# Kernel tuning notes

Measured on AMD Instinct MI355X. Metric: run time of the kernel, lower is better.

The kernel has to match this reference:

```python
import jax, jax.numpy as jnp
import numpy as np

N_EMBED = 1024
N_HEADS = 16
HEAD = N_EMBED // N_HEADS
EPS = 1e-5


def setup_inputs() -> dict:
    key = jax.random.key(0)
    ks = jax.random.split(key, 16)
    C = N_EMBED
    s = lambda fan_in: 1.0 / np.sqrt(fan_in)
    return {
        "x": jax.random.normal(ks[0], (4, 2048, C), jnp.float32),
        "ln1_g": jnp.ones((C,), jnp.float32),
        "ln1_b": jnp.zeros((C,), jnp.float32),
        "w_attn": jax.random.normal(ks[1], (C, 3 * C), jnp.float32) * s(C),
        "b_attn": jnp.zeros((3 * C,), jnp.float32),
        "w_proj": jax.random.normal(ks[2], (C, C), jnp.float32) * s(C),
        "b_proj": jnp.zeros((C,), jnp.float32),
        "ln2_g": jnp.ones((C,), jnp.float32),
        "ln2_b": jnp.zeros((C,), jnp.float32),
        "w_fc": jax.random.normal(ks[3], (C, 4 * C), jnp.float32) * s(C),
        "b_fc": jnp.zeros((4 * C,), jnp.float32),
        "w_fc2": jax.random.normal(ks[4], (4 * C, C), jnp.float32) * s(4 * C),
        "b_fc2": jnp.zeros((C,), jnp.float32),
    }


def _layernorm(x, g, b):
    mu = jnp.mean(x, axis=-1, keepdims=True)
    var = jnp.mean(jnp.square(x - mu), axis=-1, keepdims=True)
    return (x - mu) * jax.lax.rsqrt(var + EPS) * g + b


def _attention(x, w_attn, b_attn, w_proj, b_proj):
    B, T, C = x.shape
    qkv = x @ w_attn + b_attn  # [B,T,3C]
    q, k, v = jnp.split(qkv, 3, axis=-1)
    q = q.reshape(B, T, N_HEADS, HEAD).transpose(0, 2, 1, 3)  # [B,H,T,D]
    k = k.reshape(B, T, N_HEADS, HEAD).transpose(0, 2, 1, 3)
    v = v.reshape(B, T, N_HEADS, HEAD).transpose(0, 2, 1, 3)
    scale = 1.0 / np.sqrt(HEAD)
    affin = jnp.einsum("bhqd,bhkd->bhqk", q, k) * scale  # [B,H,T,T]
    causal = jnp.tril(jnp.ones((T, T), bool))
    affin = jnp.where(causal, affin, -jnp.inf)
    affin = jax.nn.softmax(affin, axis=-1)
    y = jnp.einsum("bhqk,bhkd->bhqd", affin, v)  # [B,H,T,D]
    y = y.transpose(0, 2, 1, 3).reshape(B, T, C)
    return y @ w_proj + b_proj


def reference(x, ln1_g, ln1_b, w_attn, b_attn, w_proj, b_proj,
              ln2_g, ln2_b, w_fc, b_fc, w_fc2, b_fc2):
    x = x + _attention(_layernorm(x, ln1_g, ln1_b), w_attn, b_attn, w_proj, b_proj)
    h = _layernorm(x, ln2_g, ln2_b)
    h = jax.nn.gelu(h @ w_fc + b_fc, approximate=True)  # tanh GELU
    x = x + (h @ w_fc2 + b_fc2)
    return x
```

## Files before the change

kernel.cpp:

```cpp
#include <hip/hip_runtime.h>
#include <math.h>


#define M_ROWS 8192
#define T_SEQ 2048
#define N_EMB 1024
#define N_HEADS 16
#define HEAD_D 64

typedef _Float16 f16;
typedef __attribute__((ext_vector_type(8))) _Float16 f16x8;
typedef __attribute__((ext_vector_type(4))) _Float16 f16x4;
typedef __attribute__((ext_vector_type(4))) float f32x4;

__device__ __forceinline__ void async16(void* lds, const void* g) {
    __builtin_amdgcn_global_load_lds(
        (const __attribute__((address_space(1))) unsigned int*)g,
        (__attribute__((address_space(3))) unsigned int*)lds, 16, 0, 0);
}

__device__ __forceinline__ float gelu_tanh(float v) {
    float u = 0.7978845608028654f * (v + 0.044715f * v * v * v);
    float e = __expf(2.0f * u);
    float t = 1.0f - 2.0f / (e + 1.0f);
    return 0.5f * v * (1.0f + t);
}

__launch_bounds__(256)
__global__ void wconv_kernel(const float* __restrict__ W, f16* __restrict__ WT,
                             int K, int N) {
    __shared__ float t[32][33];
    int tx = threadIdx.x & 31, ty = threadIdx.x >> 5;
    int n0 = blockIdx.x * 32, k0 = blockIdx.y * 32;
    #pragma unroll
    for (int r = 0; r < 4; r++)
        t[ty * 4 + r][tx] = W[(size_t)(k0 + ty * 4 + r) * N + n0 + tx];
    __syncthreads();
    #pragma unroll
    for (int r = 0; r < 4; r++)
        WT[(size_t)(n0 + ty * 4 + r) * K + k0 + tx] = (f16)t[tx][ty * 4 + r];
}

__launch_bounds__(256)
__global__ void ln_kernel(const float* __restrict__ x, const float* __restrict__ g,
                          const float* __restrict__ b, f16* __restrict__ y) {
    int row = blockIdx.x;
    int tid = threadIdx.x;
    const float* xr = x + (size_t)row * N_EMB;
    float4 v = *(const float4*)(xr + tid * 4);
    float s  = v.x + v.y + v.z + v.w;
    float sq = v.x * v.x + v.y * v.y + v.z * v.z + v.w * v.w;
    #pragma unroll
    for (int off = 32; off > 0; off >>= 1) {
        s  += __shfl_down(s, off);
        sq += __shfl_down(sq, off);
    }
    __shared__ float ws_[4], wq_[4];
    __shared__ float mean_s, rstd_s;
    int lane = tid & 63, wid = tid >> 6;
    if (lane == 0) { ws_[wid] = s; wq_[wid] = sq; }
    __syncthreads();
    if (tid == 0) {
        float st = ws_[0] + ws_[1] + ws_[2] + ws_[3];
        float qt = wq_[0] + wq_[1] + wq_[2] + wq_[3];
        float mu = st * (1.0f / N_EMB);
        float var = qt * (1.0f / N_EMB) - mu * mu;
        mean_s = mu;
        rstd_s = rsqrtf(var + 1e-5f);
    }
    __syncthreads();
    float mu = mean_s, r = rstd_s;
    float4 gv = *(const float4*)(g + tid * 4);
    float4 bv = *(const float4*)(b + tid * 4);
    f16x4 o;
    o.x = (f16)((v.x - mu) * r * gv.x + bv.x);
    o.y = (f16)((v.y - mu) * r * gv.y + bv.y);
    o.z = (f16)((v.z - mu) * r * gv.z + bv.z);
    o.w = (f16)((v.w - mu) * r * gv.w + bv.w);
    *(f16x4*)(y + (size_t)row * N_EMB + tid * 4) = o;
}

template <int EPI>
__launch_bounds__(256)
__global__ void gemm_f16(const f16* __restrict__ A, const f16* __restrict__ Bt,
                         const float* __restrict__ bias, const float* __restrict__ res,
                         float* __restrict__ Cf, f16* __restrict__ Ch,
                         f16* __restrict__ vT, int K, int N) {
    __shared__ f16 As[128 * 32];
    __shared__ f16 Bs[128 * 32];
    int tid = threadIdx.x;
    int lane = tid & 63, wave = tid >> 6;
    int wr = wave >> 1, wc = wave & 1;
    int quad = lane >> 4, l16 = lane & 15;
    int m0 = blockIdx.y * 128, n0 = blockIdx.x * 128;

    f32x4 acc[4][4] = {};

    for (int k0 = 0; k0 < K; k0 += 32) {
        #pragma unroll
        for (int i = 0; i < 2; i++) {
            int L = i * 256 + tid;
            int row = L >> 2, seg = L & 3;
            async16((char*)As + (size_t)L * 16,
                    A + (size_t)(m0 + row) * K + k0 + seg * 8);
        }
        #pragma unroll
        for (int i = 0; i < 2; i++) {
            int L = i * 256 + tid;
            int row = L >> 2, seg = L & 3;
            async16((char*)Bs + (size_t)L * 16,
                    Bt + (size_t)(n0 + row) * K + k0 + seg * 8);
        }
        __syncthreads();

        f16x8 af[4], bf[4];
        #pragma unroll
        for (int i = 0; i < 4; i++)
            af[i] = *(const f16x8*)&As[(wr * 64 + i * 16 + l16) * 32 + quad * 8];
        #pragma unroll
        for (int j = 0; j < 4; j++)
            bf[j] = *(const f16x8*)&Bs[(wc * 64 + j * 16 + l16) * 32 + quad * 8];
        #pragma unroll
        for (int i = 0; i < 4; i++)
            #pragma unroll
            for (int j = 0; j < 4; j++)
                acc[i][j] = __builtin_amdgcn_mfma_f32_16x16x32_f16(
                    af[i], bf[j], acc[i][j], 0, 0, 0);
        __syncthreads();
    }

    #pragma unroll
    for (int i = 0; i < 4; i++) {
        int row0 = m0 + wr * 64 + i * 16 + quad * 4;
        #pragma unroll
        for (int j = 0; j < 4; j++) {
            int col = n0 + wc * 64 + j * 16 + l16;
            float bb = bias[col];
            if (EPI == 3) {
                if (n0 < 2048) {
                    #pragma unroll
                    for (int r = 0; r < 4; r++)
                        Ch[(size_t)(row0 + r) * 2048 + col] = (f16)(acc[i][j][r] + bb);
                } else {
                    int hh = (col - 2048) >> 6, dd = col & 63;
                    int bb_ = row0 >> 11, t0 = row0 & 2047;
                    f16x4 pk;
                    pk.x = (f16)(acc[i][j][0] + bb);
                    pk.y = (f16)(acc[i][j][1] + bb);
                    pk.z = (f16)(acc[i][j][2] + bb);
                    pk.w = (f16)(acc[i][j][3] + bb);
                    *(f16x4*)(vT + ((size_t)(bb_ * 16 + hh) * 64 + dd) * 2048 + t0) = pk;
                }
            } else {
                #pragma unroll
                for (int r = 0; r < 4; r++) {
                    size_t idx = (size_t)(row0 + r) * N + col;
                    float v = acc[i][j][r] + bb;
                    if (EPI == 1) v += res[idx];
                    if (EPI == 2) Ch[idx] = (f16)gelu_tanh(v);
                    else          Cf[idx] = v;
                }
            }
        }
    }
}

__launch_bounds__(256, 2)
__global__ void flash_kernel(const f16* __restrict__ qk, const f16* __restrict__ vT,
                             f16* __restrict__ y) {
    __shared__ __align__(16) char smem[67584];
    f16* Ks = (f16*)smem;
    f16* Vs = (f16*)(smem + 16384);
    int tid = threadIdx.x;
    int lane = tid & 63, w = tid >> 6;
    int quad = lane >> 4, l16 = lane & 15;
    f16* Ps = (f16*)(smem + 32768 + w * 8704);

    int qt = 15 - blockIdx.x;
    int bh = blockIdx.y;
    int b = bh >> 4, h = bh & 15;
    int q0 = qt * 128;

    f16x8 qf[2][2];
    #pragma unroll
    for (int qn = 0; qn < 2; qn++) {
        int q = q0 + w * 32 + qn * 16 + l16;
        #pragma unroll
        for (int dblk = 0; dblk < 2; dblk++)
            qf[qn][dblk] = *(const f16x8*)(qk + (size_t)(b * T_SEQ + q) * 2048 +
                                           h * 64 + dblk * 32 + quad * 8);
    }

    float m_r[2] = {-INFINITY, -INFINITY};
    float l_r[2] = {0.0f, 0.0f};
    f32x4 Oacc[2][4] = {};
    const float scale = 0.125f;

    for (int jt = 0; jt <= qt; jt++) {
        int j0 = jt * 128;
        __syncthreads();
        #pragma unroll
        for (int i = 0; i < 4; i++) {
            int L = i * 256 + tid;
            int j = L >> 3, g1 = L & 7;
            int g = g1 ^ (j & 7);
            async16((char*)Ks + (size_t)L * 16,
                    qk + (size_t)(b * T_SEQ + j0 + j) * 2048 + 1024 + h * 64 + g * 8);
        }
        #pragma unroll
        for (int i = 0; i < 4; i++) {
            int L = i * 256 + tid;
            int d = L >> 4, g1 = L & 15;
            int g = (g1 & 8) | ((g1 ^ d) & 7);
            async16((char*)Vs + (size_t)L * 16,
                    vT + ((size_t)(bh) * 64 + d) * 2048 + j0 + g * 8);
        }
        __syncthreads();

        f32x4 S[8][2];
        #pragma unroll
        for (int jm = 0; jm < 8; jm++) {
            f16x8 kf[2];
            #pragma unroll
            for (int dblk = 0; dblk < 2; dblk++) {
                int j = jm * 16 + l16;
                int g = (dblk * 4 + quad) ^ (j & 7);
                kf[dblk] = *(const f16x8*)(Ks + (size_t)(j * 8 + g) * 8);
            }
            #pragma unroll
            for (int qn = 0; qn < 2; qn++) {
                f32x4 s = {};
                s = __builtin_amdgcn_mfma_f32_16x16x32_f16(kf[0], qf[qn][0], s, 0, 0, 0);
                s = __builtin_amdgcn_mfma_f32_16x16x32_f16(kf[1], qf[qn][1], s, 0, 0, 0);
                S[jm][qn] = s;
            }
        }

        if (jt == qt) {
            #pragma unroll
            for (int jm = 0; jm < 8; jm++)
                #pragma unroll
                for (int qn = 0; qn < 2; qn++)
                    #pragma unroll
                    for (int r = 0; r < 4; r++) {
                        int jl = jm * 16 + quad * 4 + r;
                        int ql = w * 32 + qn * 16 + l16;
                        if (jl > ql) S[jm][qn][r] = -1e30f;
                    }
        }

        float alpha[2];
        #pragma unroll
        for (int qn = 0; qn < 2; qn++) {
            float tmax = -INFINITY;
            #pragma unroll
            for (int jm = 0; jm < 8; jm++)
                #pragma unroll
                for (int r = 0; r < 4; r++)
                    tmax = fmaxf(tmax, S[jm][qn][r]);
            tmax = fmaxf(tmax, __shfl_xor(tmax, 16));
            tmax = fmaxf(tmax, __shfl_xor(tmax, 32));
            tmax *= scale;
            float mnew = fmaxf(m_r[qn], tmax);
            alpha[qn] = __expf(m_r[qn] - mnew);
            m_r[qn] = mnew;
            float rsum = 0.0f;
            #pragma unroll
            for (int jm = 0; jm < 8; jm++)
                #pragma unroll
                for (int r = 0; r < 4; r++) {
                    float p = __expf(S[jm][qn][r] * scale - mnew);
                    S[jm][qn][r] = p;
                    rsum += p;
                }
            rsum += __shfl_xor(rsum, 16);
            rsum += __shfl_xor(rsum, 32);
            l_r[qn] = l_r[qn] * alpha[qn] + rsum;
        }

        #pragma unroll
        for (int jm = 0; jm < 8; jm++)
            #pragma unroll
            for (int qn = 0; qn < 2; qn++) {
                f16x4 pk;
                pk.x = (f16)S[jm][qn][0];
                pk.y = (f16)S[jm][qn][1];
                pk.z = (f16)S[jm][qn][2];
                pk.w = (f16)S[jm][qn][3];
                *(f16x4*)(Ps + (size_t)(qn * 16 + l16) * 136 + jm * 16 + quad * 4) = pk;
            }

        float aPV[2][4];
        #pragma unroll
        for (int m = 0; m < 2; m++)
            #pragma unroll
            for (int r = 0; r < 4; r++)
                aPV[m][r] = __shfl(alpha[m], quad * 20 + r);
        #pragma unroll
        for (int m = 0; m < 2; m++)
            #pragma unroll
            for (int n = 0; n < 4; n++)
                #pragma unroll
                for (int r = 0; r < 4; r++)
                    Oacc[m][n][r] *= aPV[m][r];

        #pragma unroll
        for (int kblk = 0; kblk < 4; kblk++) {
            f16x8 pf[2];
            #pragma unroll
            for (int m = 0; m < 2; m++)
                pf[m] = *(const f16x8*)(Ps + (size_t)(m * 16 + l16) * 136 +
                                        kblk * 32 + quad * 8);
            f16x8 vf[4];
            #pragma unroll
            for (int n = 0; n < 4; n++) {
                int d = n * 16 + l16;
                int g = (kblk * 4 + quad);
                int gs = (g & 8) | ((g ^ d) & 7);
                vf[n] = *(const f16x8*)(Vs + (size_t)(d * 16 + gs) * 8);
            }
            #pragma unroll
            for (int m = 0; m < 2; m++)
                #pragma unroll
                for (int n = 0; n < 4; n++)
                    Oacc[m][n] = __builtin_amdgcn_mfma_f32_16x16x32_f16(
                        pf[m], vf[n], Oacc[m][n], 0, 0, 0);
        }
    }

    #pragma unroll
    for (int m = 0; m < 2; m++) {
        float lPV[4];
        #pragma unroll
        for (int r = 0; r < 4; r++)
            lPV[r] = 1.0f / __shfl(l_r[m], quad * 20 + r);
        #pragma unroll
        for (int n = 0; n < 4; n++) {
            #pragma unroll
            for (int r = 0; r < 4; r++) {
                int q = q0 + w * 32 + m * 16 + quad * 4 + r;
                y[(size_t)(b * T_SEQ + q) * N_EMB + h * 64 + n * 16 + l16] =
                    (f16)(Oacc[m][n][r] * lPV[r]);
            }
        }
    }
}

extern "C" void kernel_launch(void* const* d_in, const int* in_sizes, int n_in,
                              void* d_out, int out_size, void* d_ws, size_t ws_size,
                              hipStream_t stream) {
    const float* x      = (const float*)d_in[0];
    const float* ln1_g  = (const float*)d_in[1];
    const float* ln1_b  = (const float*)d_in[2];
    const float* w_attn = (const float*)d_in[3];
    const float* b_attn = (const float*)d_in[4];
    const float* w_proj = (const float*)d_in[5];
    const float* b_proj = (const float*)d_in[6];
    const float* ln2_g  = (const float*)d_in[7];
    const float* ln2_b  = (const float*)d_in[8];
    const float* w_fc   = (const float*)d_in[9];
    const float* b_fc   = (const float*)d_in[10];
    const float* w_fc2  = (const float*)d_in[11];
    const float* b_fc2  = (const float*)d_in[12];
    float* out = (float*)d_out;

    const size_t MB = 1024 * 1024;
    char* ws = (char*)d_ws;
    f16*   lnbuf = (f16*)ws;
    f16*   qkbuf = (f16*)(ws + 16 * MB);
    f16*   vTbuf = (f16*)(ws + 48 * MB);
    f16*   ybuf  = (f16*)(ws + 64 * MB);
    f16*   h     = (f16*)(ws + 80 * MB);
    f16*   wT    = (f16*)(ws + 144 * MB);
    f16* wT_attn = wT;
    f16* wT_proj = wT_attn + (size_t)3072 * 1024;
    f16* wT_fc   = wT_proj + (size_t)1024 * 1024;
    f16* wT_fc2  = wT_fc   + (size_t)1024 * 4096;

    wconv_kernel<<<dim3(3072 / 32, 1024 / 32), 256, 0, stream>>>(w_attn, wT_attn, 1024, 3072);
    wconv_kernel<<<dim3(1024 / 32, 1024 / 32), 256, 0, stream>>>(w_proj, wT_proj, 1024, 1024);
    wconv_kernel<<<dim3(4096 / 32, 1024 / 32), 256, 0, stream>>>(w_fc,   wT_fc,   1024, 4096);
    wconv_kernel<<<dim3(1024 / 32, 4096 / 32), 256, 0, stream>>>(w_fc2,  wT_fc2,  4096, 1024);

    ln_kernel<<<M_ROWS, 256, 0, stream>>>(x, ln1_g, ln1_b, lnbuf);
    gemm_f16<3><<<dim3(3072 / 128, M_ROWS / 128), 256, 0, stream>>>(
        lnbuf, wT_attn, b_attn, nullptr, nullptr, qkbuf, vTbuf, 1024, 3072);
    flash_kernel<<<dim3(16, 64), 256, 0, stream>>>(qkbuf, vTbuf, ybuf);
    gemm_f16<1><<<dim3(1024 / 128, M_ROWS / 128), 256, 0, stream>>>(
        ybuf, wT_proj, b_proj, x, out, nullptr, nullptr, 1024, 1024);
    ln_kernel<<<M_ROWS, 256, 0, stream>>>(out, ln2_g, ln2_b, lnbuf);
    gemm_f16<2><<<dim3(4096 / 128, M_ROWS / 128), 256, 0, stream>>>(
        lnbuf, wT_fc, b_fc, nullptr, nullptr, h, nullptr, 1024, 4096);
    gemm_f16<1><<<dim3(1024 / 128, M_ROWS / 128), 256, 0, stream>>>(
        h, wT_fc2, b_fc2, out, out, nullptr, nullptr, 4096, 1024);
}
```

Before: 609.6 us.

## Swizzle GEMM LDS tiles, transpose MFMA output for vector epilogue, prescale Q

New measurement: 639.7 us. 4.9% more time.

```diff
diff --git a/kernel.cpp b/kernel.cpp
--- a/kernel.cpp
+++ b/kernel.cpp
@@ -96,70 +96,85 @@
 
     f32x4 acc[4][4] = {};
 
+    int srowA[2], ssegA[2];
+    #pragma unroll
+    for (int i = 0; i < 2; i++) {
+        int L = i * 256 + tid;
+        int row = L >> 2, seg = L & 3;
+        srowA[i] = row;
+        ssegA[i] = seg ^ (row & 3) ^ ((row >> 2) & 3);
+    }
+    int r2 = (l16 & 3) ^ (l16 >> 2);
+
     for (int k0 = 0; k0 < K; k0 += 32) {
         #pragma unroll
         for (int i = 0; i < 2; i++) {
             int L = i * 256 + tid;
-            int row = L >> 2, seg = L & 3;
             async16((char*)As + (size_t)L * 16,
-                    A + (size_t)(m0 + row) * K + k0 + seg * 8);
+                    A + (size_t)(m0 + srowA[i]) * K + k0 + ssegA[i] * 8);
         }
         #pragma unroll
         for (int i = 0; i < 2; i++) {
             int L = i * 256 + tid;
-            int row = L >> 2, seg = L & 3;
             async16((char*)Bs + (size_t)L * 16,
-                    Bt + (size_t)(n0 + row) * K + k0 + seg * 8);
+                    Bt + (size_t)(n0 + srowA[i]) * K + k0 + ssegA[i] * 8);
         }
         __syncthreads();
 
         f16x8 af[4], bf[4];
         #pragma unroll
         for (int i = 0; i < 4; i++)
-            af[i] = *(const f16x8*)&As[(wr * 64 + i * 16 + l16) * 32 + quad * 8];
+            af[i] = *(const f16x8*)&As[(size_t)((wr * 64 + i * 16 + l16) * 4 +
+                                                (quad ^ r2)) * 8];
         #pragma unroll
         for (int j = 0; j < 4; j++)
-            bf[j] = *(const f16x8*)&Bs[(wc * 64 + j * 16 + l16) * 32 + quad * 8];
+            bf[j] = *(const f16x8*)&Bs[(size_t)((wc * 64 + j * 16 + l16) * 4 +
+                                                (quad ^ r2)) * 8];
         #pragma unroll
         for (int i = 0; i < 4; i++)
             #pragma unroll
             for (int j = 0; j < 4; j++)
                 acc[i][j] = __builtin_amdgcn_mfma_f32_16x16x32_f16(
-                    af[i], bf[j], acc[i][j], 0, 0, 0);
+                    bf[j], af[i], acc[i][j], 0, 0, 0);
         __syncthreads();
     }
 
     #pragma unroll
     for (int i = 0; i < 4; i++) {
-        int row0 = m0 + wr * 64 + i * 16 + quad * 4;
+        int m = m0 + wr * 64 + i * 16 + l16;
         #pragma unroll
         for (int j = 0; j < 4; j++) {
-            int col = n0 + wc * 64 + j * 16 + l16;
-            float bb = bias[col];
+            int nb = n0 + wc * 64 + j * 16 + quad * 4;
+            float4 bb = *(const float4*)(bias + nb);
+            float v0 = acc[i][j][0] + bb.x;
+            float v1 = acc[i][j][1] + bb.y;
+            float v2 = acc[i][j][2] + bb.z;
+            float v3 = acc[i][j][3] + bb.w;
             if (EPI == 3) {
                 if (n0 < 2048) {
-                    #pragma unroll
-                    for (int r = 0; r < 4; r++)
-                        Ch[(size_t)(row0 + r) * 2048 + col] = (f16)(acc[i][j][r] + bb);
+                    f16x4 pk = {(f16)v0, (f16)v1, (f16)v2, (f16)v3};
+                    *(f16x4*)(Ch + (size_t)m * 2048 + nb) = pk;
                 } else {
-                    int hh = (col - 2048) >> 6, dd = col & 63;
-                    int bb_ = row0 >> 11, t0 = row0 & 2047;
-                    f16x4 pk;
-                    pk.x = (f16)(acc[i][j][0] + bb);
-                    pk.y = (f16)(acc[i][j][1] + bb);
-                    pk.z = (f16)(acc[i][j][2] + bb);
-                    pk.w = (f16)(acc[i][j][3] + bb);
-                    *(f16x4*)(vT + ((size_t)(bb_ * 16 + hh) * 64 + dd) * 2048 + t0) = pk;
+                    int hh = (nb - 2048) >> 6, d0 = nb & 63;
+                    int b_ = m >> 11, t0 = m & 2047;
+                    f16* vbase = vT + ((size_t)(b_ * 16 + hh) * 64 + d0) * 2048 + t0;
+                    vbase[0]        = (f16)v0;
+                    vbase[2048]     = (f16)v1;
+                    vbase[2 * 2048] = (f16)v2;
+                    vbase[3 * 2048] = (f16)v3;
                 }
+            } else if (EPI == 2) {
+                f16x4 pk = {(f16)gelu_tanh(v0), (f16)gelu_tanh(v1),
+                            (f16)gelu_tanh(v2), (f16)gelu_tanh(v3)};
+                *(f16x4*)(Ch + (size_t)m * N + nb) = pk;
             } else {
-                #pragma unroll
-                for (int r = 0; r < 4; r++) {
-                    size_t idx = (size_t)(row0 + r) * N + col;
-                    float v = acc[i][j][r] + bb;
-                    if (EPI == 1) v += res[idx];
-                    if (EPI == 2) Ch[idx] = (f16)gelu_tanh(v);
-                    else          Cf[idx] = v;
+                size_t idx = (size_t)m * N + nb;
+                if (EPI == 1) {
+                    float4 rr = *(const float4*)(res + idx);
+                    v0 += rr.x; v1 += rr.y; v2 += rr.z; v3 += rr.w;
                 }
+                float4 ov = {v0, v1, v2, v3};
+                *(float4*)(Cf + idx) = ov;
             }
         }
     }
@@ -186,15 +201,18 @@
     for (int qn = 0; qn < 2; qn++) {
         int q = q0 + w * 32 + qn * 16 + l16;
         #pragma unroll
-        for (int dblk = 0; dblk < 2; dblk++)
-            qf[qn][dblk] = *(const f16x8*)(qk + (size_t)(b * T_SEQ + q) * 2048 +
-                                           h * 64 + dblk * 32 + quad * 8);
+        for (int dblk = 0; dblk < 2; dblk++) {
+            f16x8 t = *(const f16x8*)(qk + (size_t)(b * T_SEQ + q) * 2048 +
+                                      h * 64 + dblk * 32 + quad * 8);
+            #pragma unroll
+            for (int e = 0; e < 8; e++) t[e] = t[e] * (f16)0.125f;
+            qf[qn][dblk] = t;
+        }
     }
 
     float m_r[2] = {-INFINITY, -INFINITY};
     float l_r[2] = {0.0f, 0.0f};
     f32x4 Oacc[2][4] = {};
-    const float scale = 0.125f;
 
     for (int jt = 0; jt <= qt; jt++) {
         int j0 = jt * 128;
@@ -260,7 +278,6 @@
                     tmax = fmaxf(tmax, S[jm][qn][r]);
             tmax = fmaxf(tmax, __shfl_xor(tmax, 16));
             tmax = fmaxf(tmax, __shfl_xor(tmax, 32));
-            tmax *= scale;
             float mnew = fmaxf(m_r[qn], tmax);
             alpha[qn] = __expf(m_r[qn] - mnew);
             m_r[qn] = mnew;
@@ -269,7 +286,7 @@
             for (int jm = 0; jm < 8; jm++)
                 #pragma unroll
                 for (int r = 0; r < 4; r++) {
-                    float p = __expf(S[jm][qn][r] * scale - mnew);
+                    float p = __expf(S[jm][qn][r] - mnew);
                     S[jm][qn][r] = p;
                     rsum += p;
                 }
```

## Double-buffer GEMM LDS tiles and fold attention scale into Q

Applied to the files above, without the earlier changes.

Result: faster. 576.5 us (-5.4%).

```diff
diff --git a/kernel.cpp b/kernel.cpp
--- a/kernel.cpp
+++ b/kernel.cpp
@@ -86,47 +86,56 @@
                          const float* __restrict__ bias, const float* __restrict__ res,
                          float* __restrict__ Cf, f16* __restrict__ Ch,
                          f16* __restrict__ vT, int K, int N) {
-    __shared__ f16 As[128 * 32];
-    __shared__ f16 Bs[128 * 32];
+    __shared__ f16 As[2][128 * 32];
+    __shared__ f16 Bs[2][128 * 32];
     int tid = threadIdx.x;
     int lane = tid & 63, wave = tid >> 6;
     int wr = wave >> 1, wc = wave & 1;
     int quad = lane >> 4, l16 = lane & 15;
     int m0 = blockIdx.y * 128, n0 = blockIdx.x * 128;
 
+    int r0 = tid >> 2;
+    int s0 = (tid & 3) * 8;
+    const f16* paA0 = A  + (size_t)(m0 + r0) * K + s0;
+    const f16* paA1 = A  + (size_t)(m0 + r0 + 64) * K + s0;
+    const f16* paB0 = Bt + (size_t)(n0 + r0) * K + s0;
+    const f16* paB1 = Bt + (size_t)(n0 + r0 + 64) * K + s0;
+    char* dA0 = (char*)As + (size_t)tid * 16;
+    char* dA1 = (char*)As + (size_t)(256 + tid) * 16;
+    char* dB0 = (char*)Bs + (size_t)tid * 16;
+    char* dB1 = (char*)Bs + (size_t)(256 + tid) * 16;
+
+    async16(dA0, paA0);
+    async16(dA1, paA1);
+    async16(dB0, paB0);
+    async16(dB1, paB1);
+
     f32x4 acc[4][4] = {};
-
-    for (int k0 = 0; k0 < K; k0 += 32) {
-        #pragma unroll
-        for (int i = 0; i < 2; i++) {
-            int L = i * 256 + tid;
-            int row = L >> 2, seg = L & 3;
-            async16((char*)As + (size_t)L * 16,
-                    A + (size_t)(m0 + row) * K + k0 + seg * 8);
-        }
-        #pragma unroll
-        for (int i = 0; i < 2; i++) {
-            int L = i * 256 + tid;
-            int row = L >> 2, seg = L & 3;
-            async16((char*)Bs + (size_t)L * 16,
-                    Bt + (size_t)(n0 + row) * K + k0 + seg * 8);
-        }
+    int p = 0;
+    for (int k0 = 0; k0 < K; k0 += 32, p ^= 1) {
         __syncthreads();
-
+        if (k0 + 32 < K) {
+            int koff = k0 + 32;
+            async16(dA0 + (p ^ 1) * 8192, paA0 + koff);
+            async16(dA1 + (p ^ 1) * 8192, paA1 + koff);
+            async16(dB0 + (p ^ 1) * 8192, paB0 + koff);
+            async16(dB1 + (p ^ 1) * 8192, paB1 + koff);
+        }
+        const f16* as = As[p];
+        const f16* bs = Bs[p];
         f16x8 af[4], bf[4];
         #pragma unroll
         for (int i = 0; i < 4; i++)
-            af[i] = *(const f16x8*)&As[(wr * 64 + i * 16 + l16) * 32 + quad * 8];
+            af[i] = *(const f16x8*)&as[(wr * 64 + i * 16 + l16) * 32 + quad * 8];
         #pragma unroll
         for (int j = 0; j < 4; j++)
-            bf[j] = *(const f16x8*)&Bs[(wc * 64 + j * 16 + l16) * 32 + quad * 8];
+            bf[j] = *(const f16x8*)&bs[(wc * 64 + j * 16 + l16) * 32 + quad * 8];
         #pragma unroll
         for (int i = 0; i < 4; i++)
             #pragma unroll
             for (int j = 0; j < 4; j++)
                 acc[i][j] = __builtin_amdgcn_mfma_f32_16x16x32_f16(
                     af[i], bf[j], acc[i][j], 0, 0, 0);
-        __syncthreads();
     }
 
     #pragma unroll
@@ -186,15 +195,18 @@
     for (int qn = 0; qn < 2; qn++) {
         int q = q0 + w * 32 + qn * 16 + l16;
         #pragma unroll
-        for (int dblk = 0; dblk < 2; dblk++)
-            qf[qn][dblk] = *(const f16x8*)(qk + (size_t)(b * T_SEQ + q) * 2048 +
-                                           h * 64 + dblk * 32 + quad * 8);
+        for (int dblk = 0; dblk < 2; dblk++) {
+            f16x8 t = *(const f16x8*)(qk + (size_t)(b * T_SEQ + q) * 2048 +
+                                      h * 64 + dblk * 32 + quad * 8);
+            #pragma unroll
+            for (int e = 0; e < 8; e++) t[e] = t[e] * (f16)0.125f;
+            qf[qn][dblk] = t;
+        }
     }
 
     float m_r[2] = {-INFINITY, -INFINITY};
     float l_r[2] = {0.0f, 0.0f};
     f32x4 Oacc[2][4] = {};
-    const float scale = 0.125f;
 
     for (int jt = 0; jt <= qt; jt++) {
         int j0 = jt * 128;
@@ -260,7 +272,6 @@
                     tmax = fmaxf(tmax, S[jm][qn][r]);
             tmax = fmaxf(tmax, __shfl_xor(tmax, 16));
             tmax = fmaxf(tmax, __shfl_xor(tmax, 32));
-            tmax *= scale;
             float mnew = fmaxf(m_r[qn], tmax);
             alpha[qn] = __expf(m_r[qn] - mnew);
             m_r[qn] = mnew;
@@ -269,7 +280,7 @@
             for (int jm = 0; jm < 8; jm++)
                 #pragma unroll
                 for (int r = 0; r < 4; r++) {
-                    float p = __expf(S[jm][qn][r] * scale - mnew);
+                    float p = __expf(S[jm][qn][r] - mnew);
                     S[jm][qn][r] = p;
                     rsum += p;
                 }
```
